# Kernel tuning notes

Hardware: AMD Instinct MI355X
Metric: run time of the kernel (lower is better)

Reference implementation:

```python
import jax, jax.numpy as jnp
import numpy as np

NEG_SLOPE = 0.2  # PyG GATConv default LeakyReLU slope


def setup_inputs() -> dict:
    key = jax.random.key(0)
    k1, k2, k3, k4, k5 = jax.random.split(key, 5)
    N, E, IN, OUT, H = 50000, 500000, 256, 64, 8
    x = jax.random.normal(k1, (N, IN), dtype=jnp.float32)
    edge_index = jax.random.randint(k2, (2, E), 0, N, dtype=jnp.int64)
    W = jax.random.normal(k3, (H, IN, OUT), dtype=jnp.float32) / np.sqrt(IN)
    a_src = jax.random.normal(k4, (H, OUT), dtype=jnp.float32) * 0.1
    a_dst = jax.random.normal(k5, (H, OUT), dtype=jnp.float32) * 0.1
    b = jnp.zeros((H, OUT), dtype=jnp.float32)
    return {"x": x, "edge_index": edge_index, "W": W, "a_src": a_src, "a_dst": a_dst, "b": b}


def reference(x, edge_index, W, a_src, a_dst, b):
    N = x.shape[0]
    # PyG GATConv default add_self_loops=True
    loops = jnp.arange(N, dtype=edge_index.dtype)
    ei = jnp.concatenate([edge_index, jnp.stack([loops, loops])], axis=1)
    src, dst = ei[0], ei[1]

    def head(Wh, ash, adh, bh):
        xp = x @ Wh                       # [N, OUT]
        als = xp @ ash                    # [N] source attention logits
        ald = xp @ adh                    # [N] dest attention logits
        e = jax.nn.leaky_relu(als[src] + ald[dst], NEG_SLOPE)  # [E+N]
        # numerically-stable segment softmax over incoming edges of each dst
        m = jnp.full((N,), -jnp.inf, dtype=e.dtype).at[dst].max(e)
        ex = jnp.exp(e - m[dst])
        denom = jax.ops.segment_sum(ex, dst, num_segments=N)
        alpha = ex / denom[dst]           # self-loops guarantee denom > 0
        out = jax.ops.segment_sum(alpha[:, None] * xp[src], dst, num_segments=N)
        return out + bh

    # vmap over the 8 independent single-head GATConvs -> [H, N, OUT]
    return jax.vmap(head)(W, a_src, a_dst, b)
```

## Files before the change

kernel.cpp:

```cpp
#include <hip/hip_runtime.h>
#include <math.h>

#define HEADS 8
#define DOUT 64
#define DIN 256
#define HC 512
#define NEG_SLOPE 0.2f

typedef __bf16 bf16;
typedef __bf16 bf16x8 __attribute__((ext_vector_type(8)));
typedef float f32x4 __attribute__((ext_vector_type(4)));

__device__ __forceinline__ float lrelu(float v) { return v > 0.f ? v : NEG_SLOPE * v; }
__device__ __forceinline__ float bflo(unsigned u) { return __uint_as_float(u << 16); }
__device__ __forceinline__ float bfhi(unsigned u) { return __uint_as_float(u & 0xffff0000u); }

__device__ __forceinline__ void fma8x2(float* acc, uint4 u, float w0, float w1) {
    acc[0] += w0 * bflo(u.x); acc[1] += w0 * bfhi(u.x);
    acc[2] += w0 * bflo(u.y); acc[3] += w0 * bfhi(u.y);
    acc[4] += w1 * bflo(u.z); acc[5] += w1 * bfhi(u.z);
    acc[6] += w1 * bflo(u.w); acc[7] += w1 * bfhi(u.w);
}

__global__ void wprep_kernel(const float* __restrict__ W, bf16* __restrict__ Wt) {
    int idx = blockIdx.x * 256 + threadIdx.x;
    int h = idx >> 14, rem = idx & 16383, k = rem >> 6, c = rem & 63;
    Wt[(((size_t)h * 64 + c) << 8) + k] = (bf16)W[idx];
}

__global__ __launch_bounds__(256) void gemm_kernel(const float* __restrict__ x,
                                                   const bf16* __restrict__ Wt,
                                                   bf16* __restrict__ xpb,
                                                   const float* __restrict__ a_src,
                                                   const float* __restrict__ a_dst,
                                                   float* __restrict__ als,
                                                   float* __restrict__ ald, int N) {
    __shared__ bf16 Alds[128 * 40];
    __shared__ bf16 Blds[128 * 40];

    int m0 = blockIdx.x * 128;
    int colbase = blockIdx.y * 128;

    int t = threadIdx.x;
    int wv = t >> 6, lane = t & 63, quad = lane >> 4, l16 = lane & 15;
    int k8 = quad * 8;

    f32x4 acc[2][8] = {};

    for (int kt = 0; kt < DIN; kt += 32) {
        {
            int m = t >> 1, half = t & 1;
            int row = m0 + m;
            bf16 tmp[16];
            if (row < N) {
                const float* sp = x + (size_t)row * DIN + kt + half * 16;
                float4 v0 = *(const float4*)(sp + 0);
                float4 v1 = *(const float4*)(sp + 4);
                float4 v2 = *(const float4*)(sp + 8);
                float4 v3 = *(const float4*)(sp + 12);
                tmp[0] = (bf16)v0.x; tmp[1] = (bf16)v0.y; tmp[2] = (bf16)v0.z; tmp[3] = (bf16)v0.w;
                tmp[4] = (bf16)v1.x; tmp[5] = (bf16)v1.y; tmp[6] = (bf16)v1.z; tmp[7] = (bf16)v1.w;
                tmp[8] = (bf16)v2.x; tmp[9] = (bf16)v2.y; tmp[10] = (bf16)v2.z; tmp[11] = (bf16)v2.w;
                tmp[12] = (bf16)v3.x; tmp[13] = (bf16)v3.y; tmp[14] = (bf16)v3.z; tmp[15] = (bf16)v3.w;
            } else {
#pragma unroll
                for (int i = 0; i < 16; i++) tmp[i] = (bf16)0.f;
            }
            *(uint4*)&Alds[m * 40 + half * 16] = *(uint4*)&tmp[0];
            *(uint4*)&Alds[m * 40 + half * 16 + 8] = *(uint4*)&tmp[8];
        }
#pragma unroll
        for (int i = 0; i < 2; i++) {
            int e = t + 256 * i;
            int c = e >> 2, seg = e & 3;
            const bf16* sp = Wt + (size_t)(colbase + c) * DIN + kt + seg * 8;
            *(uint4*)&Blds[c * 40 + seg * 8] = *(const uint4*)sp;
        }
        __syncthreads();

        bf16x8 af0 = *(bf16x8*)&Alds[(wv * 32 + l16) * 40 + k8];
        bf16x8 af1 = *(bf16x8*)&Alds[(wv * 32 + 16 + l16) * 40 + k8];
#pragma unroll
        for (int c = 0; c < 8; c++) {
            bf16x8 bf = *(bf16x8*)&Blds[(c * 16 + l16) * 40 + k8];
            acc[0][c] = __builtin_amdgcn_mfma_f32_16x16x32_bf16(af0, bf, acc[0][c], 0, 0, 0);
            acc[1][c] = __builtin_amdgcn_mfma_f32_16x16x32_bf16(af1, bf, acc[1][c], 0, 0, 0);
        }
        __syncthreads();
    }

    int h0 = colbase >> 6;
    float as8[8], ad8[8];
#pragma unroll
    for (int c = 0; c < 8; c++) {
        as8[c] = a_src[colbase + c * 16 + l16];
        ad8[c] = a_dst[colbase + c * 16 + l16];
    }
#pragma unroll
    for (int s = 0; s < 2; s++) {
        float ls[2][4] = {}, ldd[2][4] = {};
#pragma unroll
        for (int c = 0; c < 8; c++)
#pragma unroll
            for (int r = 0; r < 4; r++) {
                float v = acc[s][c][r];
                ls[c >> 2][r] += v * as8[c];
                ldd[c >> 2][r] += v * ad8[c];
            }
#pragma unroll
        for (int d = 1; d < 16; d <<= 1)
#pragma unroll
            for (int hh = 0; hh < 2; hh++)
#pragma unroll
                for (int r = 0; r < 4; r++) {
                    ls[hh][r] += __shfl_xor(ls[hh][r], d);
                    ldd[hh][r] += __shfl_xor(ldd[hh][r], d);
                }
        if (l16 == 0) {
#pragma unroll
            for (int hh = 0; hh < 2; hh++)
#pragma unroll
                for (int r = 0; r < 4; r++) {
                    int row = m0 + wv * 32 + s * 16 + quad * 4 + r;
                    if (row < N) {
                        als[row * HEADS + h0 + hh] = ls[hh][r];
                        ald[row * HEADS + h0 + hh] = ldd[hh][r];
                    }
                }
        }
#pragma unroll
        for (int r = 0; r < 4; r++) {
            int row = m0 + wv * 32 + s * 16 + quad * 4 + r;
            if (row < N) {
                bf16 t8[8];
#pragma unroll
                for (int c = 0; c < 8; c++) t8[c] = (bf16)acc[s][c][r];
                *(uint4*)&xpb[(size_t)row * HC + colbase + l16 * 8] = *(uint4*)t8;
            }
        }
    }
}

__global__ void deg_kernel(const int* __restrict__ dst, int* __restrict__ deg, int E) {
    int i = blockIdx.x * blockDim.x + threadIdx.x;
    if (i < E) atomicAdd(&deg[dst[i]], 1);
}

__global__ __launch_bounds__(256) void scan_sums(const int* __restrict__ deg,
                                                 int* __restrict__ bsum, int N) {
    int i = blockIdx.x * 256 + threadIdx.x;
    int v = (i < N) ? deg[i] : 0;
#pragma unroll
    for (int d = 32; d > 0; d >>= 1) v += __shfl_xor(v, d);
    __shared__ int p[4];
    if ((threadIdx.x & 63) == 0) p[threadIdx.x >> 6] = v;
    __syncthreads();
    if (threadIdx.x == 0) bsum[blockIdx.x] = p[0] + p[1] + p[2] + p[3];
}

__global__ __launch_bounds__(256) void scan_boffs(const int* __restrict__ bsum,
                                                  int* __restrict__ boffs, int NB) {
    int t = threadIdx.x, wid = t >> 6, lane = t & 63;
    int orig = (t < NB) ? bsum[t] : 0;
    int v = orig;
#pragma unroll
    for (int d = 1; d < 64; d <<= 1) {
        int y = __shfl_up(v, d);
        if (lane >= d) v += y;
    }
    __shared__ int wt[4];
    if (lane == 63) wt[wid] = v;
    __syncthreads();
    int add = 0;
#pragma unroll
    for (int ww = 0; ww < 4; ww++)
        if (ww < wid) add += wt[ww];
    v += add;
    if (t < NB) boffs[t] = v - orig;
}

__global__ __launch_bounds__(256) void scan_offs(const int* __restrict__ deg,
                                                 const int* __restrict__ boffs,
                                                 int* __restrict__ offs, int N) {
    int bI = blockIdx.x, t = threadIdx.x, wid = t >> 6, lane = t & 63;
    int i = bI * 256 + t;
    int orig = (i < N) ? deg[i] : 0;
    int v = orig;
#pragma unroll
    for (int d = 1; d < 64; d <<= 1) {
        int y = __shfl_up(v, d);
        if (lane >= d) v += y;
    }
    __shared__ int wt[4];
    if (lane == 63) wt[wid] = v;
    __syncthreads();
    int add = 0;
#pragma unroll
    for (int ww = 0; ww < 4; ww++)
        if (ww < wid) add += wt[ww];
    int incl = v + add;
    int base = boffs[bI];
    if (i < N) offs[i] = base + incl - orig;
    if (i == N - 1) offs[N] = base + incl;
}

__global__ void fill_kernel(const int* __restrict__ src, const int* __restrict__ dst,
                            const int* __restrict__ offs, int* __restrict__ deg,
                            int* __restrict__ csr, int E) {
    int i = blockIdx.x * blockDim.x + threadIdx.x;
    if (i < E) {
        int d = dst[i];
        int pos = offs[d] + atomicSub(&deg[d], 1) - 1;
        csr[pos] = src[i];
    }
}

__global__ __launch_bounds__(256) void agg_kernel(const bf16* __restrict__ xp,
                                                  const float* __restrict__ als,
                                                  const float* __restrict__ ald,
                                                  const int* __restrict__ offs,
                                                  const int* __restrict__ csr,
                                                  const float* __restrict__ bias,
                                                  float* __restrict__ out, int N) {
    int n = blockIdx.x * 4 + (threadIdx.x >> 6);
    if (n >= N) return;
    int lane = threadIdx.x & 63;
    int hp = lane >> 4, l16 = lane & 15;

    float2 aldn = *(const float2*)&ald[n * HEADS + hp * 2];
    float2 alsn = *(const float2*)&als[n * HEADS + hp * 2];
    float es0 = lrelu(alsn.x + aldn.x);
    float es1 = lrelu(alsn.y + aldn.y);

    int start = offs[n];
    int deg = offs[n + 1] - start;

    float acc[8];
    {
        uint4 u = *(const uint4*)&xp[(size_t)n * HC + lane * 8];
        acc[0] = bflo(u.x); acc[1] = bfhi(u.x);
        acc[2] = bflo(u.y); acc[3] = bfhi(u.y);
        acc[4] = bflo(u.z); acc[5] = bfhi(u.z);
        acc[6] = bflo(u.w); acc[7] = bfhi(u.w);
    }
    float d0 = 1.f, d1 = 1.f;

    for (int c0 = 0; c0 < deg; c0 += 64) {
        int cnt = min(64, deg - c0);
        int sreg = (lane < cnt) ? csr[start + c0 + lane] : 0;
        int jj = 0;
        for (; jj + 4 <= cnt; jj += 4) {
            int s0 = __shfl(sreg, jj), s1 = __shfl(sreg, jj + 1);
            int s2 = __shfl(sreg, jj + 2), s3 = __shfl(sreg, jj + 3);
            float2 a0 = *(const float2*)&als[s0 * HEADS + hp * 2];
            float2 a1 = *(const float2*)&als[s1 * HEADS + hp * 2];
            float2 a2 = *(const float2*)&als[s2 * HEADS + hp * 2];
            float2 a3 = *(const float2*)&als[s3 * HEADS + hp * 2];
            uint4 u0 = *(const uint4*)&xp[(size_t)s0 * HC + lane * 8];
            uint4 u1 = *(const uint4*)&xp[(size_t)s1 * HC + lane * 8];
            uint4 u2 = *(const uint4*)&xp[(size_t)s2 * HC + lane * 8];
            uint4 u3 = *(const uint4*)&xp[(size_t)s3 * HC + lane * 8];
            float w00 = __expf(lrelu(a0.x + aldn.x) - es0), w01 = __expf(lrelu(a0.y + aldn.y) - es1);
            float w10 = __expf(lrelu(a1.x + aldn.x) - es0), w11 = __expf(lrelu(a1.y + aldn.y) - es1);
            float w20 = __expf(lrelu(a2.x + aldn.x) - es0), w21 = __expf(lrelu(a2.y + aldn.y) - es1);
            float w30 = __expf(lrelu(a3.x + aldn.x) - es0), w31 = __expf(lrelu(a3.y + aldn.y) - es1);
            fma8x2(acc, u0, w00, w01); d0 += w00; d1 += w01;
            fma8x2(acc, u1, w10, w11); d0 += w10; d1 += w11;
            fma8x2(acc, u2, w20, w21); d0 += w20; d1 += w21;
            fma8x2(acc, u3, w30, w31); d0 += w30; d1 += w31;
        }
        for (; jj < cnt; jj++) {
            int s0 = __shfl(sreg, jj);
            float2 a0 = *(const float2*)&als[s0 * HEADS + hp * 2];
            uint4 u0 = *(const uint4*)&xp[(size_t)s0 * HC + lane * 8];
            float w00 = __expf(lrelu(a0.x + aldn.x) - es0), w01 = __expf(lrelu(a0.y + aldn.y) - es1);
            fma8x2(acc, u0, w00, w01); d0 += w00; d1 += w01;
        }
    }

    float i0 = 1.f / d0, i1 = 1.f / d1;
    size_t ob0 = (size_t)(hp * 2) * N * DOUT + (size_t)n * DOUT + l16;
    size_t ob1 = ob0 + (size_t)N * DOUT;
    int bb0 = (hp * 2) * DOUT + l16, bb1 = bb0 + DOUT;
#pragma unroll
    for (int c = 0; c < 4; c++) {
        out[ob0 + c * 16] = acc[c] * i0 + bias[bb0 + c * 16];
        out[ob1 + c * 16] = acc[c + 4] * i1 + bias[bb1 + c * 16];
    }
}

extern "C" void kernel_launch(void* const* d_in, const int* in_sizes, int n_in,
                              void* d_out, int out_size, void* d_ws, size_t ws_size,
                              hipStream_t stream) {
    const float* x = (const float*)d_in[0];
    const int* ei = (const int*)d_in[1];
    const float* W = (const float*)d_in[2];
    const float* a_src = (const float*)d_in[3];
    const float* a_dst = (const float*)d_in[4];
    const float* b = (const float*)d_in[5];
    float* out = (float*)d_out;

    int N = in_sizes[0] / DIN;
    int E = in_sizes[1] / 2;
    const int* src = ei;
    const int* dst = ei + E;
    int NB = (N + 255) / 256;

    bf16* xpb = (bf16*)d_ws;
    float* als = (float*)(xpb + (size_t)N * HC);
    float* ald = als + (size_t)N * HEADS;
    bf16* Wt = (bf16*)(ald + (size_t)N * HEADS);
    int* deg = (int*)(Wt + HEADS * DIN * DOUT);
    int* offs = deg + N;
    int* bsum = offs + N + 1;
    int* boffs = bsum + 256;
    int* csr = boffs + 256;

    (void)hipMemsetAsync(deg, 0, (size_t)N * sizeof(int), stream);

    wprep_kernel<<<(HEADS * DIN * DOUT) / 256, 256, 0, stream>>>(W, Wt);
    dim3 ggrid((N + 127) / 128, HEADS / 2);
    gemm_kernel<<<ggrid, 256, 0, stream>>>(x, Wt, xpb, a_src, a_dst, als, ald, N);
    deg_kernel<<<(E + 255) / 256, 256, 0, stream>>>(dst, deg, E);
    scan_sums<<<NB, 256, 0, stream>>>(deg, bsum, N);
    scan_boffs<<<1, 256, 0, stream>>>(bsum, boffs, NB);
    scan_offs<<<NB, 256, 0, stream>>>(deg, boffs, offs, N);
    fill_kernel<<<(E + 255) / 256, 256, 0, stream>>>(src, dst, offs, deg, csr, E);
    agg_kernel<<<(N + 3) / 4, 256, 0, stream>>>(xpb, als, ald, offs, csr, b, out, N);
}
```

Before: 339.8 us.

## Widen GEMM column tile, pre-convert x to bf16, batch aggregation gathers

Result: slower. 388.3 us (+14.3%).

```diff
diff --git a/kernel.cpp b/kernel.cpp
--- a/kernel.cpp
+++ b/kernel.cpp
@@ -28,49 +28,74 @@
     Wt[(((size_t)h * 64 + c) << 8) + k] = (bf16)W[idx];
 }
 
+__global__ __launch_bounds__(256) void xprep_kernel(const float* __restrict__ x,
+                                                    bf16* __restrict__ xb, int total8) {
+    int i = blockIdx.x * 256 + threadIdx.x;
+    if (i >= total8) return;
+    const float4* xp4 = (const float4*)x;
+    float4 v0 = xp4[(size_t)i * 2];
+    float4 v1 = xp4[(size_t)i * 2 + 1];
+    bf16 t8[8] = {(bf16)v0.x, (bf16)v0.y, (bf16)v0.z, (bf16)v0.w,
+                  (bf16)v1.x, (bf16)v1.y, (bf16)v1.z, (bf16)v1.w};
+    *(uint4*)&xb[(size_t)i * 8] = *(uint4*)t8;
+}
+
 __global__ __launch_bounds__(256) void gemm_kernel(const float* __restrict__ x,
+                                                   const bf16* __restrict__ xb,
                                                    const bf16* __restrict__ Wt,
                                                    bf16* __restrict__ xpb,
                                                    const float* __restrict__ a_src,
                                                    const float* __restrict__ a_dst,
                                                    float* __restrict__ als,
-                                                   float* __restrict__ ald, int N) {
+                                                   float* __restrict__ ald, int N, int use_xb) {
     __shared__ bf16 Alds[128 * 40];
-    __shared__ bf16 Blds[128 * 40];
+    __shared__ bf16 Blds[256 * 40];
 
     int m0 = blockIdx.x * 128;
-    int colbase = blockIdx.y * 128;
+    int colbase = blockIdx.y * 256;
 
     int t = threadIdx.x;
     int wv = t >> 6, lane = t & 63, quad = lane >> 4, l16 = lane & 15;
     int k8 = quad * 8;
 
-    f32x4 acc[2][8] = {};
+    f32x4 acc[2][16] = {};
 
     for (int kt = 0; kt < DIN; kt += 32) {
         {
             int m = t >> 1, half = t & 1;
             int row = m0 + m;
-            bf16 tmp[16];
-            if (row < N) {
-                const float* sp = x + (size_t)row * DIN + kt + half * 16;
-                float4 v0 = *(const float4*)(sp + 0);
-                float4 v1 = *(const float4*)(sp + 4);
-                float4 v2 = *(const float4*)(sp + 8);
-                float4 v3 = *(const float4*)(sp + 12);
-                tmp[0] = (bf16)v0.x; tmp[1] = (bf16)v0.y; tmp[2] = (bf16)v0.z; tmp[3] = (bf16)v0.w;
-                tmp[4] = (bf16)v1.x; tmp[5] = (bf16)v1.y; tmp[6] = (bf16)v1.z; tmp[7] = (bf16)v1.w;
-                tmp[8] = (bf16)v2.x; tmp[9] = (bf16)v2.y; tmp[10] = (bf16)v2.z; tmp[11] = (bf16)v2.w;
-                tmp[12] = (bf16)v3.x; tmp[13] = (bf16)v3.y; tmp[14] = (bf16)v3.z; tmp[15] = (bf16)v3.w;
+            if (use_xb) {
+                if (row < N) {
+                    const bf16* sp = xb + (size_t)row * DIN + kt + half * 16;
+                    *(uint4*)&Alds[m * 40 + half * 16] = *(const uint4*)sp;
+                    *(uint4*)&Alds[m * 40 + half * 16 + 8] = *(const uint4*)(sp + 8);
+                } else {
+                    uint4 z = make_uint4(0, 0, 0, 0);
+                    *(uint4*)&Alds[m * 40 + half * 16] = z;
+                    *(uint4*)&Alds[m * 40 + half * 16 + 8] = z;
+                }
             } else {
-#pragma unroll
-                for (int i = 0; i < 16; i++) tmp[i] = (bf16)0.f;
+                bf16 tmp[16];
+                if (row < N) {
+                    const float* sp = x + (size_t)row * DIN + kt + half * 16;
+                    float4 v0 = *(const float4*)(sp + 0);
+                    float4 v1 = *(const float4*)(sp + 4);
+                    float4 v2 = *(const float4*)(sp + 8);
+                    float4 v3 = *(const float4*)(sp + 12);
+                    tmp[0] = (bf16)v0.x; tmp[1] = (bf16)v0.y; tmp[2] = (bf16)v0.z; tmp[3] = (bf16)v0.w;
+                    tmp[4] = (bf16)v1.x; tmp[5] = (bf16)v1.y; tmp[6] = (bf16)v1.z; tmp[7] = (bf16)v1.w;
+                    tmp[8] = (bf16)v2.x; tmp[9] = (bf16)v2.y; tmp[10] = (bf16)v2.z; tmp[11] = (bf16)v2.w;
+                    tmp[12] = (bf16)v3.x; tmp[13] = (bf16)v3.y; tmp[14] = (bf16)v3.z; tmp[15] = (bf16)v3.w;
+                } else {
+#pragma unroll
+                    for (int i = 0; i < 16; i++) tmp[i] = (bf16)0.f;
+                }
+                *(uint4*)&Alds[m * 40 + half * 16] = *(uint4*)&tmp[0];
+                *(uint4*)&Alds[m * 40 + half * 16 + 8] = *(uint4*)&tmp[8];
             }
-            *(uint4*)&Alds[m * 40 + half * 16] = *(uint4*)&tmp[0];
-            *(uint4*)&Alds[m * 40 + half * 16 + 8] = *(uint4*)&tmp[8];
-        }
-#pragma unroll
-        for (int i = 0; i < 2; i++) {
+        }
+#pragma unroll
+        for (int i = 0; i < 4; i++) {
             int e = t + 256 * i;
             int c = e >> 2, seg = e & 3;
             const bf16* sp = Wt + (size_t)(colbase + c) * DIN + kt + seg * 8;
@@ -81,36 +106,36 @@
         bf16x8 af0 = *(bf16x8*)&Alds[(wv * 32 + l16) * 40 + k8];
         bf16x8 af1 = *(bf16x8*)&Alds[(wv * 32 + 16 + l16) * 40 + k8];
 #pragma unroll
-        for (int c = 0; c < 8; c++) {
-            bf16x8 bf = *(bf16x8*)&Blds[(c * 16 + l16) * 40 + k8];
-            acc[0][c] = __builtin_amdgcn_mfma_f32_16x16x32_bf16(af0, bf, acc[0][c], 0, 0, 0);
-            acc[1][c] = __builtin_amdgcn_mfma_f32_16x16x32_bf16(af1, bf, acc[1][c], 0, 0, 0);
+        for (int c = 0; c < 16; c++) {
+            bf16x8 bfg = *(bf16x8*)&Blds[(c * 16 + l16) * 40 + k8];
+            acc[0][c] = __builtin_amdgcn_mfma_f32_16x16x32_bf16(af0, bfg, acc[0][c], 0, 0, 0);
+            acc[1][c] = __builtin_amdgcn_mfma_f32_16x16x32_bf16(af1, bfg, acc[1][c], 0, 0, 0);
         }
         __syncthreads();
     }
 
     int h0 = colbase >> 6;
-    float as8[8], ad8[8];
-#pragma unroll
-    for (int c = 0; c < 8; c++) {
-        as8[c] = a_src[colbase + c * 16 + l16];
-        ad8[c] = a_dst[colbase + c * 16 + l16];
+    float as16[16], ad16[16];
+#pragma unroll
+    for (int c = 0; c < 16; c++) {
+        as16[c] = a_src[colbase + c * 16 + l16];
+        ad16[c] = a_dst[colbase + c * 16 + l16];
     }
 #pragma unroll
     for (int s = 0; s < 2; s++) {
-        float ls[2][4] = {}, ldd[2][4] = {};
-#pragma unroll
-        for (int c = 0; c < 8; c++)
+        float ls[4][4] = {}, ldd[4][4] = {};
+#pragma unroll
+        for (int c = 0; c < 16; c++)
 #pragma unroll
             for (int r = 0; r < 4; r++) {
                 float v = acc[s][c][r];
-                ls[c >> 2][r] += v * as8[c];
-                ldd[c >> 2][r] += v * ad8[c];
+                ls[c >> 2][r] += v * as16[c];
+                ldd[c >> 2][r] += v * ad16[c];
             }
 #pragma unroll
         for (int d = 1; d < 16; d <<= 1)
 #pragma unroll
-            for (int hh = 0; hh < 2; hh++)
+            for (int hh = 0; hh < 4; hh++)
 #pragma unroll
                 for (int r = 0; r < 4; r++) {
                     ls[hh][r] += __shfl_xor(ls[hh][r], d);
@@ -118,7 +143,7 @@
                 }
         if (l16 == 0) {
 #pragma unroll
-            for (int hh = 0; hh < 2; hh++)
+            for (int hh = 0; hh < 4; hh++)
 #pragma unroll
                 for (int r = 0; r < 4; r++) {
                     int row = m0 + wv * 32 + s * 16 + quad * 4 + r;
@@ -132,10 +157,13 @@
         for (int r = 0; r < 4; r++) {
             int row = m0 + wv * 32 + s * 16 + quad * 4 + r;
             if (row < N) {
-                bf16 t8[8];
+                bf16 t8[8], t8b[8];
 #pragma unroll
                 for (int c = 0; c < 8; c++) t8[c] = (bf16)acc[s][c][r];
+#pragma unroll
+                for (int c = 0; c < 8; c++) t8b[c] = (bf16)acc[s][c + 8][r];
                 *(uint4*)&xpb[(size_t)row * HC + colbase + l16 * 8] = *(uint4*)t8;
+                *(uint4*)&xpb[(size_t)row * HC + colbase + 128 + l16 * 8] = *(uint4*)t8b;
             }
         }
     }
@@ -248,33 +276,28 @@
     for (int c0 = 0; c0 < deg; c0 += 64) {
         int cnt = min(64, deg - c0);
         int sreg = (lane < cnt) ? csr[start + c0 + lane] : 0;
-        int jj = 0;
-        for (; jj + 4 <= cnt; jj += 4) {
-            int s0 = __shfl(sreg, jj), s1 = __shfl(sreg, jj + 1);
-            int s2 = __shfl(sreg, jj + 2), s3 = __shfl(sreg, jj + 3);
-            float2 a0 = *(const float2*)&als[s0 * HEADS + hp * 2];
-            float2 a1 = *(const float2*)&als[s1 * HEADS + hp * 2];
-            float2 a2 = *(const float2*)&als[s2 * HEADS + hp * 2];
-            float2 a3 = *(const float2*)&als[s3 * HEADS + hp * 2];
-            uint4 u0 = *(const uint4*)&xp[(size_t)s0 * HC + lane * 8];
-            uint4 u1 = *(const uint4*)&xp[(size_t)s1 * HC + lane * 8];
-            uint4 u2 = *(const uint4*)&xp[(size_t)s2 * HC + lane * 8];
-            uint4 u3 = *(const uint4*)&xp[(size_t)s3 * HC + lane * 8];
-            float w00 = __expf(lrelu(a0.x + aldn.x) - es0), w01 = __expf(lrelu(a0.y + aldn.y) - es1);
-            float w10 = __expf(lrelu(a1.x + aldn.x) - es0), w11 = __expf(lrelu(a1.y + aldn.y) - es1);
-            float w20 = __expf(lrelu(a2.x + aldn.x) - es0), w21 = __expf(lrelu(a2.y + aldn.y) - es1);
-            float w30 = __expf(lrelu(a3.x + aldn.x) - es0), w31 = __expf(lrelu(a3.y + aldn.y) - es1);
-            fma8x2(acc, u0, w00, w01); d0 += w00; d1 += w01;
-            fma8x2(acc, u1, w10, w11); d0 += w10; d1 += w11;
-            fma8x2(acc, u2, w20, w21); d0 += w20; d1 += w21;
-            fma8x2(acc, u3, w30, w31); d0 += w30; d1 += w31;
-        }
-        for (; jj < cnt; jj++) {
-            int s0 = __shfl(sreg, jj);
-            float2 a0 = *(const float2*)&als[s0 * HEADS + hp * 2];
-            uint4 u0 = *(const uint4*)&xp[(size_t)s0 * HC + lane * 8];
-            float w00 = __expf(lrelu(a0.x + aldn.x) - es0), w01 = __expf(lrelu(a0.y + aldn.y) - es1);
-            fma8x2(acc, u0, w00, w01); d0 += w00; d1 += w01;
+        for (int jj = 0; jj < cnt; jj += 8) {
+            int rem = cnt - jj;
+            int s[8];
+            float2 a[8];
+            uint4 u[8];
+#pragma unroll
+            for (int q = 0; q < 8; q++)
+                if (q < rem) s[q] = __shfl(sreg, jj + q);
+#pragma unroll
+            for (int q = 0; q < 8; q++)
+                if (q < rem) u[q] = *(const uint4*)&xp[(size_t)s[q] * HC + lane * 8];
+#pragma unroll
+            for (int q = 0; q < 8; q++)
+                if (q < rem) a[q] = *(const float2*)&als[s[q] * HEADS + hp * 2];
+#pragma unroll
+            for (int q = 0; q < 8; q++)
+                if (q < rem) {
+                    float w0 = __expf(lrelu(a[q].x + aldn.x) - es0);
+                    float w1 = __expf(lrelu(a[q].y + aldn.y) - es1);
+                    fma8x2(acc, u[q], w0, w1);
+                    d0 += w0; d1 += w1;
+                }
         }
     }
 
@@ -316,11 +339,19 @@
     int* boffs = bsum + 256;
     int* csr = boffs + 256;
 
+    bf16* xb = (bf16*)(((uintptr_t)(csr + E) + 15) & ~(uintptr_t)15);
+    size_t need = (size_t)((char*)(xb + (size_t)N * DIN) - (char*)d_ws);
+    int use_xb = (ws_size >= need) ? 1 : 0;
+
     (void)hipMemsetAsync(deg, 0, (size_t)N * sizeof(int), stream);
 
     wprep_kernel<<<(HEADS * DIN * DOUT) / 256, 256, 0, stream>>>(W, Wt);
-    dim3 ggrid((N + 127) / 128, HEADS / 2);
-    gemm_kernel<<<ggrid, 256, 0, stream>>>(x, Wt, xpb, a_src, a_dst, als, ald, N);
+    if (use_xb) {
+        int total8 = (N * DIN) / 8;
+        xprep_kernel<<<(total8 + 255) / 256, 256, 0, stream>>>(x, xb, total8);
+    }
+    dim3 ggrid((N + 127) / 128, HC / 256);
+    gemm_kernel<<<ggrid, 256, 0, stream>>>(x, xb, Wt, xpb, a_src, a_dst, als, ald, N, use_xb);
     deg_kernel<<<(E + 255) / 256, 256, 0, stream>>>(dst, deg, E);
     scan_sums<<<NB, 256, 0, stream>>>(deg, bsum, N);
     scan_boffs<<<1, 256, 0, stream>>>(bsum, boffs, NB);
```
